# Optimization experiments

Hardware: AMD Instinct MI355X
Metric: run time of the kernel (lower is better)

The kernel has to match this reference:

```python
import math
import jax, jax.numpy as jnp
import numpy as np

DIM = 2048
HID = 4 * DIM
SEQ = 2048
BATCH = 2
EPS = 1e-5


def _layernorm(x, g, b):
    mu = jnp.mean(x, axis=-1, keepdims=True)
    var = jnp.var(x, axis=-1, keepdims=True)
    return (x - mu) * jax.lax.rsqrt(var + EPS) * g + b


def setup_inputs() -> dict:
    key = jax.random.key(0)
    ks = jax.random.split(key, 12)
    s = 1.0 / math.sqrt(DIM)
    x = jax.random.normal(ks[0], (BATCH, SEQ, DIM), dtype=jnp.float32)
    # additive causal mask: 0 on/below diagonal, -1e9 above
    mask = jnp.where(jnp.tril(jnp.ones((SEQ, SEQ), dtype=bool)), 0.0, -1e9).astype(jnp.float32)
    freqs_cis = jax.random.normal(ks[1], (SEQ, 64), dtype=jnp.float32)  # unused by forward
    return {
        "x": x,
        "mask": mask,
        "start_pos": 0,
        "freqs_cis": freqs_cis,
        "wq": jax.random.normal(ks[2], (DIM, DIM), dtype=jnp.float32) * s,
        "bq": jnp.zeros((DIM,), dtype=jnp.float32),
        "wk": jax.random.normal(ks[3], (DIM, DIM), dtype=jnp.float32) * s,
        "bk": jnp.zeros((DIM,), dtype=jnp.float32),
        "wv": jax.random.normal(ks[4], (DIM, DIM), dtype=jnp.float32) * s,
        "bv": jnp.zeros((DIM,), dtype=jnp.float32),
        "g_ln1": jnp.ones((DIM,), dtype=jnp.float32),
        "b_ln1": jnp.zeros((DIM,), dtype=jnp.float32),
        "g_ln2": jnp.ones((DIM,), dtype=jnp.float32),
        "b_ln2": jnp.zeros((DIM,), dtype=jnp.float32),
        "w1": jax.random.normal(ks[5], (DIM, HID), dtype=jnp.float32) * s,
        "b1": jnp.zeros((HID,), dtype=jnp.float32),
        "w2": jax.random.normal(ks[6], (HID, DIM), dtype=jnp.float32) * (1.0 / math.sqrt(HID)),
        "b2": jnp.zeros((DIM,), dtype=jnp.float32),
    }


def reference(x, mask, start_pos, freqs_cis, wq, bq, wk, bk, wv, bv,
              g_ln1, b_ln1, g_ln2, b_ln2, w1, b1, w2, b2):
    # pre-norm attention (no head split; scale by sqrt(full dim); dropout=eval identity)
    h = _layernorm(x, g_ln1, b_ln1)
    q = h @ wq + bq
    k = h @ wk + bk
    v = h @ wv + bv
    scores = jnp.einsum('bqd,bkd->bqk', q, k) / math.sqrt(DIM) + mask
    attn = jax.nn.softmax(scores, axis=-1)
    attn_out = jnp.einsum('bqk,bkd->bqd', attn, v)
    h2 = _layernorm(x + attn_out, g_ln2, b_ln2)
    ffn = jax.nn.gelu(h2 @ w1 + b1, approximate=False) @ w2 + b2
    # NOTE: original code adds FFN output to the ORIGINAL x (attn residual dropped here)
    return x + ffn
```

## Files before the change

kernel.cpp:

```cpp
#include <hip/hip_runtime.h>
#include <math.h>

#define DIM_ 2048
#define HID_ 8192
#define SEQ_ 2048
#define BATCH_ 2
#define TOK_ (BATCH_*SEQ_)

typedef __attribute__((ext_vector_type(4))) float f32x4;
typedef __attribute__((ext_vector_type(8))) __bf16 bf16x8;
typedef __attribute__((ext_vector_type(4))) unsigned int u32x4;
typedef __attribute__((ext_vector_type(4))) short s16x4;
typedef __attribute__((ext_vector_type(8))) short s16x8;
typedef __attribute__((address_space(3))) short* lds_sp;

__device__ __forceinline__ short f2bf(float f) {
  union { float f; unsigned u; } v; v.f = f;
  unsigned r = v.u + 0x7FFFu + ((v.u >> 16) & 1u);
  return (short)(r >> 16);
}
__device__ __forceinline__ float bf2f(short s) {
  union { unsigned u; float f; } v; v.u = ((unsigned)(unsigned short)s) << 16;
  return v.f;
}

__device__ __forceinline__ f32x4 mfma16(u32x4 a, u32x4 b, f32x4 c) {
  return __builtin_amdgcn_mfma_f32_16x16x32_bf16(
      __builtin_bit_cast(bf16x8, a), __builtin_bit_cast(bf16x8, b), c, 0, 0, 0);
}

#define DSR(dst, addr) asm volatile("ds_read_b128 %0, %1" : "=v"(dst) : "v"(addr))
#define BARv()  __builtin_amdgcn_s_barrier()
#define LGKM0() do { asm volatile("s_waitcnt lgkmcnt(0)" ::: "memory"); \
                     __builtin_amdgcn_sched_barrier(0); } while(0)
#define VM3()   asm volatile("s_waitcnt vmcnt(3)" ::: "memory")
#define PRIO1() __builtin_amdgcn_s_setprio(1)
#define PRIO0() __builtin_amdgcn_s_setprio(0)

#define TILE_MAP(BM, BN) \
  const int nwg  = gridDim.x * gridDim.y; \
  const int orig = blockIdx.y * gridDim.x + blockIdx.x; \
  const int wgid = (orig & 7) * (nwg >> 3) + (orig >> 3); \
  const int gy4  = (int)gridDim.y << 2; \
  const int rem  = wgid % gy4; \
  const int tn   = ((wgid / gy4) * 4 + (rem & 3)) * (BN); \
  const int tm   = (rem >> 2) * (BM);

template<int EPI>
__device__ __forceinline__ void epi_store(void* Cv, const float* bias, const float* aux,
                                          int z, long long sC, int ldc, int N,
                                          int row, int col, float v)
{
  if (EPI == 1) {
    ((float*)Cv + (long long)z * sC)[(long long)row * ldc + col] = v;
  } else if (EPI == 0) {
    v += bias[col];
    ((short*)Cv + (long long)z * sC)[(long long)row * ldc + col] = f2bf(v);
  } else if (EPI == 2) {
    v += bias[col];
    v = 0.5f * v * (1.0f + erff(v * 0.70710678118654752f));
    ((short*)Cv + (long long)z * sC)[(long long)row * ldc + col] = f2bf(v);
  } else if (EPI == 3) {
    v += bias[col] + aux[(long long)row * ldc + col];
    ((float*)Cv + (long long)z * sC)[(long long)row * ldc + col] = v;
  } else {
    v = v * 0.022097086912079608f + aux[(long long)row * ldc + col];
    ((short*)Cv + (long long)z * sC)[(long long)row * ldc + col] = f2bf(v);
  }
}

#define HRD(slot) do { \
  const unsigned a_ = aBaseH + (unsigned)(slot)*8192u; \
  const unsigned b_ = bBaseH + (unsigned)(slot)*16384u; \
  DSR(af[0], a_ + offk);          DSR(af[1], a_ + 1024u + offk); \
  DSR(af[2], a_ + 2048u + offk);  DSR(af[3], a_ + 3072u + offk); \
  DSR(bf[0], b_ + offk);          DSR(bf[1], b_ + 1024u + offk); \
  DSR(bf[2], b_ + 2048u + offk);  DSR(bf[3], b_ + 3072u + offk); \
} while(0)

#define HMM() do { \
  _Pragma("unroll") \
  for (int mi = 0; mi < 4; ++mi) \
    _Pragma("unroll") \
    for (int ni = 0; ni < 4; ++ni) \
      acc[mi][ni] = mfma16(af[mi], bf[ni], acc[mi][ni]); \
} while(0)

template<int EPI>
__global__ __launch_bounds__(512, 4)
void gemm_hi(const short* __restrict__ A, const short* __restrict__ B,
             void* __restrict__ Cv, const float* __restrict__ bias,
             const float* __restrict__ aux,
             int M, int N, int K, int lda, int ldb, int ldc,
             long long sA, long long sB, long long sC)
{
  __shared__ __align__(16) short As[3*128*32];
  __shared__ __align__(16) short Bs[3*256*32];
  const int lane = threadIdx.x & 63;
  const int wave = threadIdx.x >> 6;
  const int wr = wave >> 2, wc = wave & 3;
  TILE_MAP(128, 256)
  const int z = blockIdx.z;
  A += (long long)z * sA;
  B += (long long)z * sB;

  const int NT = K >> 5;

  const int rr   = wave * 16 + (lane >> 2);
  const int soff = (((lane & 3) ^ ((lane >> 3) & 3)) << 3);
  const short* pA = A + (long long)(tm + rr) * lda + soff;
  const short* pB = B + (long long)(tn + rr) * ldb + soff;
  const long long ldb128 = 128LL * ldb;

  auto stage = [&](int t, int slot) {
    const long long ko = (long long)t << 5;
    __builtin_amdgcn_global_load_lds(
        (const __attribute__((address_space(1))) void*)(pA + ko),
        (__attribute__((address_space(3))) void*)(As + slot * 4096 + wave * 512), 16, 0, 0);
    __builtin_amdgcn_global_load_lds(
        (const __attribute__((address_space(1))) void*)(pB + ko),
        (__attribute__((address_space(3))) void*)(Bs + slot * 8192 + wave * 512), 16, 0, 0);
    __builtin_amdgcn_global_load_lds(
        (const __attribute__((address_space(1))) void*)(pB + ldb128 + ko),
        (__attribute__((address_space(3))) void*)(Bs + slot * 8192 + 4096 + wave * 512), 16, 0, 0);
  };

  const unsigned asB = (unsigned)(unsigned long long)(lds_sp)As;
  const unsigned bsB = (unsigned)(unsigned long long)(lds_sp)Bs;
  const int l15 = lane & 15, l4 = lane >> 4;
  const unsigned offk  = (unsigned)((l4 ^ ((l15 >> 1) & 3)) << 4);
  const unsigned aBaseH = asB + (unsigned)(wr * 4096 + l15 * 64);
  const unsigned bBaseH = bsB + (unsigned)(wc * 4096 + l15 * 64);

  f32x4 acc[4][4] = {};
  u32x4 af[4], bf[4];

  stage(0, 0);
  stage(1 < NT ? 1 : 0, 1);
  VM3();
  BARv();

  int rd = 0;
  #pragma unroll 1
  for (int t = 0; t < NT; ++t) {
    const int st = rd + 2 >= 3 ? rd - 1 : rd + 2;
    const int tc = t + 2 < NT ? t + 2 : NT - 1;
    HRD(rd);
    stage(tc, st);
    BARv(); LGKM0();
    PRIO1(); HMM(); PRIO0();
    VM3();
    BARv();
    rd = rd + 1 >= 3 ? 0 : rd + 1;
  }

  const int row0 = tm + wr * 64 + l4 * 4;
  const int col0 = tn + wc * 64 + l15;
  #pragma unroll
  for (int mi = 0; mi < 4; ++mi)
    #pragma unroll
    for (int j = 0; j < 4; ++j)
      #pragma unroll
      for (int ni = 0; ni < 4; ++ni)
        epi_store<EPI>(Cv, bias, aux, z, sC, ldc, N,
                       row0 + mi * 16 + j, col0 + ni * 16, acc[mi][ni][j]);
}

__global__ __launch_bounds__(256)
void ln_kernel(const float* __restrict__ x, const float* __restrict__ res,
               const float* __restrict__ g, const float* __restrict__ b,
               short* __restrict__ out, int hasres)
{
  const int row = blockIdx.x;
  const int tid = threadIdx.x;
  const float4* X = (const float4*)x + (long long)row * 512;
  float4 v0 = X[tid], v1 = X[tid + 256];
  if (hasres) {
    const float4* R = (const float4*)res + (long long)row * 512;
    float4 r0 = R[tid], r1 = R[tid + 256];
    v0.x += r0.x; v0.y += r0.y; v0.z += r0.z; v0.w += r0.w;
    v1.x += r1.x; v1.y += r1.y; v1.z += r1.z; v1.w += r1.w;
  }
  float s1 = v0.x + v0.y + v0.z + v0.w + v1.x + v1.y + v1.z + v1.w;
  float s2 = v0.x*v0.x + v0.y*v0.y + v0.z*v0.z + v0.w*v0.w
           + v1.x*v1.x + v1.y*v1.y + v1.z*v1.z + v1.w*v1.w;
  #pragma unroll
  for (int o = 32; o > 0; o >>= 1) { s1 += __shfl_xor(s1, o); s2 += __shfl_xor(s2, o); }
  __shared__ float red[8];
  if ((tid & 63) == 0) { red[tid >> 6] = s1; red[4 + (tid >> 6)] = s2; }
  __syncthreads();
  s1 = red[0] + red[1] + red[2] + red[3];
  s2 = red[4] + red[5] + red[6] + red[7];
  const float mean = s1 * (1.0f / 2048.0f);
  const float var  = s2 * (1.0f / 2048.0f) - mean * mean;
  const float rstd = rsqrtf(var + 1e-5f);
  const float4* G  = (const float4*)g;
  const float4* Bb = (const float4*)b;
  float4 g0 = G[tid], g1 = G[tid + 256], b0 = Bb[tid], b1 = Bb[tid + 256];
  s16x4 o0, o1;
  o0[0] = f2bf((v0.x - mean) * rstd * g0.x + b0.x);
  o0[1] = f2bf((v0.y - mean) * rstd * g0.y + b0.y);
  o0[2] = f2bf((v0.z - mean) * rstd * g0.z + b0.z);
  o0[3] = f2bf((v0.w - mean) * rstd * g0.w + b0.w);
  o1[0] = f2bf((v1.x - mean) * rstd * g1.x + b1.x);
  o1[1] = f2bf((v1.y - mean) * rstd * g1.y + b1.y);
  o1[2] = f2bf((v1.z - mean) * rstd * g1.z + b1.z);
  o1[3] = f2bf((v1.w - mean) * rstd * g1.w + b1.w);
  *(s16x4*)&out[(long long)row * 2048 + tid * 4]        = o0;
  *(s16x4*)&out[(long long)row * 2048 + 1024 + tid * 4] = o1;
}

__global__ __launch_bounds__(256)
void softmax_bf16_kernel(short* __restrict__ probs)
{
  const long long row = blockIdx.x;
  const int tid = threadIdx.x;
  short* P = probs + row * 2048 + tid * 8;
  s16x8 in = *(const s16x8*)P;
  float a[8];
  #pragma unroll
  for (int i = 0; i < 8; ++i) a[i] = bf2f(in[i]);
  float mx = a[0];
  #pragma unroll
  for (int i = 1; i < 8; ++i) mx = fmaxf(mx, a[i]);
  #pragma unroll
  for (int o = 32; o > 0; o >>= 1) mx = fmaxf(mx, __shfl_xor(mx, o));
  __shared__ float red[8];
  if ((tid & 63) == 0) red[tid >> 6] = mx;
  __syncthreads();
  mx = fmaxf(fmaxf(red[0], red[1]), fmaxf(red[2], red[3]));
  float e[8], sum = 0.f;
  #pragma unroll
  for (int i = 0; i < 8; ++i) { e[i] = __expf(a[i] - mx); sum += e[i]; }
  #pragma unroll
  for (int o = 32; o > 0; o >>= 1) sum += __shfl_xor(sum, o);
  if ((tid & 63) == 0) red[4 + (tid >> 6)] = sum;
  __syncthreads();
  sum = red[4] + red[5] + red[6] + red[7];
  const float inv = 1.0f / sum;
  s16x8 o;
  #pragma unroll
  for (int i = 0; i < 8; ++i) o[i] = f2bf(e[i] * inv);
  *(s16x8*)P = o;
}

__global__ __launch_bounds__(256)
void cvt_transpose64(const float* __restrict__ in, short* __restrict__ out,
                     int R, int C)
{
  __shared__ float t[64][69];
  const int r0 = blockIdx.y << 6, c0 = blockIdx.x << 6;
  const int tx = threadIdx.x & 15, ty = threadIdx.x >> 4;
  #pragma unroll
  for (int p = 0; p < 4; ++p) {
    const int r = ty + p * 16;
    float4 v = *(const float4*)&in[(long long)(r0 + r) * C + c0 + tx * 4];
    t[r][tx*4+0] = v.x; t[r][tx*4+1] = v.y; t[r][tx*4+2] = v.z; t[r][tx*4+3] = v.w;
  }
  __syncthreads();
  #pragma unroll
  for (int p = 0; p < 4; ++p) {
    const int oc = ty + p * 16;
    s16x4 o;
    o[0] = f2bf(t[tx*4+0][oc]); o[1] = f2bf(t[tx*4+1][oc]);
    o[2] = f2bf(t[tx*4+2][oc]); o[3] = f2bf(t[tx*4+3][oc]);
    *(s16x4*)&out[(long long)(c0 + oc) * R + r0 + tx * 4] = o;
  }
}

__global__ __launch_bounds__(256)
void transpose_bf16_kernel(const short* __restrict__ in, short* __restrict__ out,
                           int ldin, int ldout, long long sin_, long long sout_)
{
  __shared__ short t[32][33];
  in  += (long long)blockIdx.z * sin_;
  out += (long long)blockIdx.z * sout_;
  const int tx = threadIdx.x & 31, ty = threadIdx.x >> 5;
  const int r0 = blockIdx.y << 5, c0 = blockIdx.x << 5;
  #pragma unroll
  for (int i = 0; i < 32; i += 8)
    t[ty + i][tx] = in[(long long)(r0 + ty + i) * ldin + c0 + tx];
  __syncthreads();
  #pragma unroll
  for (int i = 0; i < 32; i += 8)
    out[(long long)(c0 + ty + i) * ldout + r0 + tx] = t[tx][ty + i];
}

__global__ __launch_bounds__(256)
void concat_bias_kernel(const float* a, const float* b, const float* c, float* o)
{
  const int i = blockIdx.x * 256 + threadIdx.x;
  o[i] = i < 2048 ? a[i] : (i < 4096 ? b[i - 2048] : c[i - 4096]);
}

extern "C" void kernel_launch(void* const* d_in, const int* in_sizes, int n_in,
                              void* d_out, int out_size, void* d_ws, size_t ws_size,
                              hipStream_t stream)
{
  const float* x    = (const float*)d_in[0];
  const float* mask = (const float*)d_in[1];
  const float* wq   = (const float*)d_in[4];
  const float* bq   = (const float*)d_in[5];
  const float* wk   = (const float*)d_in[6];
  const float* bk   = (const float*)d_in[7];
  const float* wv   = (const float*)d_in[8];
  const float* bv   = (const float*)d_in[9];
  const float* g1   = (const float*)d_in[10];
  const float* b1   = (const float*)d_in[11];
  const float* g2   = (const float*)d_in[12];
  const float* b2   = (const float*)d_in[13];
  const float* w1   = (const float*)d_in[14];
  const float* bw1  = (const float*)d_in[15];
  const float* w2   = (const float*)d_in[16];
  const float* bw2  = (const float*)d_in[17];
  float* out = (float*)d_out;

  char* p = (char*)d_ws;
  auto take = [&](size_t bytes) { char* r = p; p += (bytes + 255) & ~(size_t)255; return r; };
  short* wqkvT = (short*)take((size_t)3 * DIM_ * DIM_ * 2);
  short* w1T   = (short*)take((size_t)DIM_ * HID_ * 2);
  short* w2T   = (short*)take((size_t)HID_ * DIM_ * 2);
  short* h_bf  = (short*)take((size_t)TOK_ * DIM_ * 2);
  short* qkv   = (short*)take((size_t)TOK_ * 3 * DIM_ * 2);
  short* vT    = (short*)take((size_t)BATCH_ * DIM_ * SEQ_ * 2);
  float* attno = (float*)take((size_t)TOK_ * DIM_ * 4);
  short* attn  = (short*)take((size_t)BATCH_ * SEQ_ * SEQ_ * 2);
  float* cbias = (float*)take((size_t)3 * DIM_ * 4);
  short* ffn1  = qkv;
  short* h2    = h_bf;

  const dim3 blk(256), gblk(512);
  cvt_transpose64<<<dim3(DIM_/64, DIM_/64), blk, 0, stream>>>(wq, wqkvT, DIM_, DIM_);
  cvt_transpose64<<<dim3(DIM_/64, DIM_/64), blk, 0, stream>>>(wk, wqkvT + (size_t)DIM_*DIM_, DIM_, DIM_);
  cvt_transpose64<<<dim3(DIM_/64, DIM_/64), blk, 0, stream>>>(wv, wqkvT + (size_t)2*DIM_*DIM_, DIM_, DIM_);
  cvt_transpose64<<<dim3(HID_/64, DIM_/64), blk, 0, stream>>>(w1, w1T, DIM_, HID_);
  cvt_transpose64<<<dim3(DIM_/64, HID_/64), blk, 0, stream>>>(w2, w2T, HID_, DIM_);
  concat_bias_kernel<<<24, blk, 0, stream>>>(bq, bk, bv, cbias);
  ln_kernel<<<TOK_, blk, 0, stream>>>(x, nullptr, g1, b1, h_bf, 0);
  gemm_hi<0><<<dim3(6144/256, TOK_/128, 1), gblk, 0, stream>>>(
      h_bf, wqkvT, qkv, cbias, nullptr, TOK_, 6144, DIM_, DIM_, DIM_, 6144, 0, 0, 0);
  gemm_hi<4><<<dim3(SEQ_/256, SEQ_/128, BATCH_), gblk, 0, stream>>>(
      qkv, qkv + DIM_, attn, nullptr, mask, SEQ_, SEQ_, DIM_, 6144, 6144, SEQ_,
      (long long)SEQ_ * 6144, (long long)SEQ_ * 6144, (long long)SEQ_ * SEQ_);
  softmax_bf16_kernel<<<BATCH_ * SEQ_, blk, 0, stream>>>(attn);
  transpose_bf16_kernel<<<dim3(DIM_/32, SEQ_/32, BATCH_), blk, 0, stream>>>(
      qkv + 2*DIM_, vT, 6144, SEQ_, (long long)SEQ_ * 6144, (long long)DIM_ * SEQ_);
  gemm_hi<1><<<dim3(DIM_/256, SEQ_/128, BATCH_), gblk, 0, stream>>>(
      attn, vT, attno, nullptr, nullptr, SEQ_, DIM_, SEQ_, SEQ_, SEQ_, DIM_,
      (long long)SEQ_ * SEQ_, (long long)DIM_ * SEQ_, (long long)SEQ_ * DIM_);
  ln_kernel<<<TOK_, blk, 0, stream>>>(x, attno, g2, b2, h2, 1);
  gemm_hi<2><<<dim3(HID_/256, TOK_/128, 1), gblk, 0, stream>>>(
      h2, w1T, ffn1, bw1, nullptr, TOK_, HID_, DIM_, DIM_, DIM_, HID_, 0, 0, 0);
  gemm_hi<3><<<dim3(DIM_/256, TOK_/128, 1), gblk, 0, stream>>>(
      ffn1, w2T, out, bw2, x, TOK_, DIM_, HID_, HID_, HID_, DIM_, 0, 0, 0);
}
```

Measured before the change: 627.5 us.

## Add 256x256-tile bf16 GEMM and use it for QKV and FFN1

Adds a new GEMM kernel with 256x256 output tiles and a three-stage LDS ring filled by direct global-to-LDS loads. The A and B loads are split across two half-steps, each interleaved with MFMA work. It replaces the 256x128 kernel for the QKV projection and the first FFN GEMM, aiming to raise arithmetic intensity and cut global/LDS traffic per flop. The cost is higher register use (8x4 accumulators) and fewer workgroups, which may lower occupancy and leave the grid with a poor tail.

```diff
diff --git a/kernel.cpp b/kernel.cpp
--- a/kernel.cpp
+++ b/kernel.cpp
@@ -34,6 +34,7 @@
 #define LGKM0() do { asm volatile("s_waitcnt lgkmcnt(0)" ::: "memory"); \
                      __builtin_amdgcn_sched_barrier(0); } while(0)
 #define VM3()   asm volatile("s_waitcnt vmcnt(3)" ::: "memory")
+#define VM4()   asm volatile("s_waitcnt vmcnt(4)" ::: "memory")
 #define PRIO1() __builtin_amdgcn_s_setprio(1)
 #define PRIO0() __builtin_amdgcn_s_setprio(0)
 
@@ -67,6 +68,120 @@
     v = v * 0.022097086912079608f + aux[(long long)row * ldc + col];
     ((short*)Cv + (long long)z * sC)[(long long)row * ldc + col] = f2bf(v);
   }
+}
+
+#define G256_RD1(slot) do { \
+  const unsigned s_ = (unsigned)(slot)*16384u; \
+  DSR(af[0], aRd + s_);          DSR(af[1], aRd + s_ + 1024u); \
+  DSR(af[2], aRd + s_ + 2048u);  DSR(af[3], aRd + s_ + 3072u); \
+  DSR(af[4], aRd + s_ + 4096u);  DSR(af[5], aRd + s_ + 5120u); \
+  DSR(af[6], aRd + s_ + 6144u);  DSR(af[7], aRd + s_ + 7168u); \
+  DSR(bf0[0], bRd + s_);         DSR(bf0[1], bRd + s_ + 1024u); \
+} while(0)
+
+#define G256_RD2(slot) do { \
+  const unsigned s_ = (unsigned)(slot)*16384u; \
+  DSR(bf1[0], bRd + s_ + 2048u); DSR(bf1[1], bRd + s_ + 3072u); \
+} while(0)
+
+#define G256_MM(c0, bA, bB) do { \
+  _Pragma("unroll") \
+  for (int fr_ = 0; fr_ < 8; ++fr_) { \
+    acc[fr_][(c0)]   = mfma16(af[fr_], bA, acc[fr_][(c0)]); \
+    acc[fr_][(c0)+1] = mfma16(af[fr_], bB, acc[fr_][(c0)+1]); \
+  } \
+} while(0)
+
+template<int EPI>
+__global__ __launch_bounds__(512, 2)
+void gemm256(const short* __restrict__ A, const short* __restrict__ B,
+             void* __restrict__ Cv, const float* __restrict__ bias,
+             const float* __restrict__ aux,
+             int M, int N, int K, int lda, int ldb, int ldc,
+             long long sA, long long sB, long long sC)
+{
+  __shared__ __align__(16) short As[3*256*32];
+  __shared__ __align__(16) short Bs[3*256*32];
+  const int lane = threadIdx.x & 63;
+  const int wave = threadIdx.x >> 6;
+  const int wr = wave >> 2, wc = wave & 3;
+  TILE_MAP(256, 256)
+  const int z = blockIdx.z;
+  A += (long long)z * sA;
+  B += (long long)z * sB;
+
+  const int NT = K >> 5;
+
+  const int rr   = wave * 16 + (lane >> 2);
+  const int soff = (((lane & 3) ^ ((lane >> 3) & 3)) << 3);
+  const short* pA = A + (long long)(tm + rr) * lda + soff;
+  const short* pB = B + (long long)(tn + rr) * ldb + soff;
+  const long long lda128 = 128LL * lda;
+  const long long ldb128 = 128LL * ldb;
+
+  auto stA = [&](int t, int slot) {
+    const long long ko = (long long)t << 5;
+    __builtin_amdgcn_global_load_lds(
+        (const __attribute__((address_space(1))) void*)(pA + ko),
+        (__attribute__((address_space(3))) void*)(As + slot * 8192 + wave * 512), 16, 0, 0);
+    __builtin_amdgcn_global_load_lds(
+        (const __attribute__((address_space(1))) void*)(pA + lda128 + ko),
+        (__attribute__((address_space(3))) void*)(As + slot * 8192 + 4096 + wave * 512), 16, 0, 0);
+  };
+  auto stB = [&](int t, int slot) {
+    const long long ko = (long long)t << 5;
+    __builtin_amdgcn_global_load_lds(
+        (const __attribute__((address_space(1))) void*)(pB + ko),
+        (__attribute__((address_space(3))) void*)(Bs + slot * 8192 + wave * 512), 16, 0, 0);
+    __builtin_amdgcn_global_load_lds(
+        (const __attribute__((address_space(1))) void*)(pB + ldb128 + ko),
+        (__attribute__((address_space(3))) void*)(Bs + slot * 8192 + 4096 + wave * 512), 16, 0, 0);
+  };
+
+  const unsigned asB = (unsigned)(unsigned long long)(lds_sp)As;
+  const unsigned bsB = (unsigned)(unsigned long long)(lds_sp)Bs;
+  const int l15 = lane & 15, l4 = lane >> 4;
+  const unsigned offk = (unsigned)((l4 ^ ((l15 >> 1) & 3)) << 4);
+  const unsigned aRd = asB + (unsigned)((wr * 128 + l15) * 64) + offk;
+  const unsigned bRd = bsB + (unsigned)((wc * 64 + l15) * 64) + offk;
+
+  f32x4 acc[8][4] = {};
+  u32x4 af[8], bf0[2], bf1[2];
+
+  stA(0, 0); stB(0, 0);
+  stA(1 < NT ? 1 : 0, 1); stB(1 < NT ? 1 : 0, 1);
+  VM4();
+  BARv();
+
+  int rd = 0;
+  #pragma unroll 1
+  for (int t = 0; t < NT; ++t) {
+    const int st = rd + 2 >= 3 ? rd - 1 : rd + 2;
+    const int tc = t + 2 < NT ? t + 2 : NT - 1;
+    G256_RD1(rd);
+    stA(tc, st);
+    BARv(); LGKM0();
+    PRIO1(); G256_MM(0, bf0[0], bf0[1]); PRIO0();
+    BARv();
+    G256_RD2(rd);
+    stB(tc, st);
+    VM4();
+    BARv(); LGKM0();
+    PRIO1(); G256_MM(2, bf1[0], bf1[1]); PRIO0();
+    BARv();
+    rd = rd + 1 >= 3 ? 0 : rd + 1;
+  }
+
+  const int row0 = tm + wr * 128 + l4 * 4;
+  const int col0 = tn + wc * 64 + l15;
+  #pragma unroll
+  for (int fr = 0; fr < 8; ++fr)
+    #pragma unroll
+    for (int j = 0; j < 4; ++j)
+      #pragma unroll
+      for (int fc = 0; fc < 4; ++fc)
+        epi_store<EPI>(Cv, bias, aux, z, sC, ldc, N,
+                       row0 + fr * 16 + j, col0 + fc * 16, acc[fr][fc][j]);
 }
 
 #define HRD(slot) do { \
@@ -337,7 +452,7 @@
   cvt_transpose64<<<dim3(DIM_/64, HID_/64), blk, 0, stream>>>(w2, w2T, HID_, DIM_);
   concat_bias_kernel<<<24, blk, 0, stream>>>(bq, bk, bv, cbias);
   ln_kernel<<<TOK_, blk, 0, stream>>>(x, nullptr, g1, b1, h_bf, 0);
-  gemm_hi<0><<<dim3(6144/256, TOK_/128, 1), gblk, 0, stream>>>(
+  gemm256<0><<<dim3(6144/256, TOK_/256, 1), gblk, 0, stream>>>(
       h_bf, wqkvT, qkv, cbias, nullptr, TOK_, 6144, DIM_, DIM_, DIM_, 6144, 0, 0, 0);
   gemm_hi<4><<<dim3(SEQ_/256, SEQ_/128, BATCH_), gblk, 0, stream>>>(
       qkv, qkv + DIM_, attn, nullptr, mask, SEQ_, SEQ_, DIM_, 6144, 6144, SEQ_,
@@ -349,7 +464,7 @@
       attn, vT, attno, nullptr, nullptr, SEQ_, DIM_, SEQ_, SEQ_, SEQ_, DIM_,
       (long long)SEQ_ * SEQ_, (long long)DIM_ * SEQ_, (long long)SEQ_ * DIM_);
   ln_kernel<<<TOK_, blk, 0, stream>>>(x, attno, g2, b2, h2, 1);
-  gemm_hi<2><<<dim3(HID_/256, TOK_/128, 1), gblk, 0, stream>>>(
+  gemm256<2><<<dim3(HID_/256, TOK_/256, 1), gblk, 0, stream>>>(
       h2, w1T, ffn1, bw1, nullptr, TOK_, HID_, DIM_, DIM_, DIM_, HID_, 0, 0, 0);
   gemm_hi<3><<<dim3(DIM_/256, TOK_/128, 1), gblk, 0, stream>>>(
       ffn1, w2T, out, bw2, x, TOK_, DIM_, HID_, HID_, HID_, DIM_, 0, 0, 0);
```

After: 638.5 us. No clear change (+1.7%).
